# Performance work log

Measured on AMD Instinct MI355X. Metric: run time of the kernel, lower is better.

Reference implementation:

```python
import jax, jax.numpy as jnp
import numpy as np

N = 16384      # nodes per graph
E = 262144     # edges per graph
D_IN = 144     # number_of_labels(16) + 128
F1, F2, F3 = 128, 64, 32
K = 16         # tensor_neurons
BINS = 16
BOTTLE = 16


def gcn_conv(x, edge_index, W, b, n):
    """PyG-style GCNConv: D^-1/2 (A+I) D^-1/2 (x W) + b."""
    h = x @ W
    loops = jnp.arange(n)
    row = jnp.concatenate([edge_index[0], loops])
    col = jnp.concatenate([edge_index[1], loops])
    deg = jax.ops.segment_sum(jnp.ones_like(row, dtype=h.dtype), row, num_segments=n)
    dinv = jax.lax.rsqrt(jnp.maximum(deg, 1e-12))
    norm = dinv[row] * dinv[col]                 # [E+N]
    msg = h[col] * norm[:, None]                 # gather + scale
    out = jax.ops.segment_sum(msg, row, num_segments=n)  # scatter-add
    return out + b


def conv_pass(edge_index, x, W1, b1, W2, b2, W3, b3, n):
    x = jax.nn.relu(gcn_conv(x, edge_index, W1, b1, n))
    x = jax.nn.relu(gcn_conv(x, edge_index, W2, b2, n))
    return gcn_conv(x, edge_index, W3, b3, n)    # [N, F3]


def attention_pool(x, att_W):
    # global context -> tanh -> sigmoid node gates -> weighted sum
    tg = jnp.tanh(jnp.mean(x @ att_W, axis=0))   # [F3]
    gates = jax.nn.sigmoid(x @ tg)               # [N]
    return (x.T @ gates)[:, None]                # [F3, 1]


def tensor_network(e1, e2, tW, tWb, tb):
    # e1, e2: [F3, 1]
    s = (e1.T @ tW.reshape(F3, -1)).reshape(F3, K)
    s = s.T @ e2                                 # [K, 1]
    blk = tWb @ jnp.concatenate([e1, e2], axis=0)  # [K, 1]
    return jax.nn.relu(s + blk + tb)


def simgnn_forward(features_1, features_2, W1, b1, W2, b2, W3, b3,
                   att_W, tnet_W, tnet_Wb, tnet_bias, fc_W, fc_b, sc_W, sc_b,
                   edge_index_1, edge_index_2):
    af1 = conv_pass(edge_index_1, features_1, W1, b1, W2, b2, W3, b3, N)
    af2 = conv_pass(edge_index_2, features_2, W1, b1, W2, b2, W3, b3, N)

    # histogram of pairwise similarity scores (detached in original)
    sim = jax.lax.stop_gradient(af1 @ af2.T)     # [N, N] -- 1 GB fp32
    counts, _ = jnp.histogram(sim.reshape(-1), bins=BINS)
    hist = (counts.astype(features_1.dtype) / counts.sum()).reshape(1, BINS)

    p1 = attention_pool(af1, att_W)
    p2 = attention_pool(af2, att_W)
    scores = tensor_network(p1, p2, tnet_W, tnet_Wb, tnet_bias).T  # [1, K]
    scores = jnp.concatenate([scores, hist], axis=1).reshape(1, -1)  # [1, K+BINS]

    scores = jax.nn.relu(scores @ fc_W.T + fc_b)
    return jax.nn.sigmoid(scores @ sc_W.T + sc_b)  # [1, 1]


def setup_inputs() -> dict:
    key = jax.random.key(0)
    ks = jax.random.split(key, 20)
    g = lambda k, shp, s: (jax.random.normal(k, shp, dtype=jnp.float32) * s)
    return {
        "features_1": jax.random.normal(ks[0], (N, D_IN), dtype=jnp.float32),
        "features_2": jax.random.normal(ks[1], (N, D_IN), dtype=jnp.float32),
        "edge_index_1": jax.random.randint(ks[2], (2, E), 0, N, dtype=jnp.int32),
        "edge_index_2": jax.random.randint(ks[3], (2, E), 0, N, dtype=jnp.int32),
        "W1": g(ks[4], (D_IN, F1), 0.08), "b1": jnp.zeros((F1,), jnp.float32),
        "W2": g(ks[5], (F1, F2), 0.09), "b2": jnp.zeros((F2,), jnp.float32),
        "W3": g(ks[6], (F2, F3), 0.12), "b3": jnp.zeros((F3,), jnp.float32),
        "att_W": g(ks[7], (F3, F3), 0.17),
        "tnet_W": g(ks[8], (F3, F3, K), 0.05),
        "tnet_Wb": g(ks[9], (K, 2 * F3), 0.1),
        "tnet_bias": g(ks[10], (K, 1), 0.1),
        "fc_W": g(ks[11], (BOTTLE, K + BINS), 0.15),
        "fc_b": jnp.zeros((BOTTLE,), jnp.float32),
        "sc_W": g(ks[12], (1, BOTTLE), 0.2),
        "sc_b": jnp.zeros((1,), jnp.float32),
    }


def reference(features_1, features_2, edge_index_1, edge_index_2,
              W1, b1, W2, b2, W3, b3, att_W, tnet_W, tnet_Wb, tnet_bias,
              fc_W, fc_b, sc_W, sc_b):
    return simgnn_forward(features_1, features_2, W1, b1, W2, b2, W3, b3,
                          att_W, tnet_W, tnet_Wb, tnet_bias, fc_W, fc_b, sc_W, sc_b,
                          edge_index_1, edge_index_2)
```

## Files before the change

### kernel.cpp

```cpp
#include <hip/hip_runtime.h>
#include <hip/hip_bf16.h>
#include <math.h>

#define NN 16384
#define EE 262144
#define DIN 144
#define F1d 128
#define F2d 64
#define F3d 32

#define SIM_BLOCKS 1024

typedef __attribute__((ext_vector_type(8))) short bf16x8;
typedef __attribute__((ext_vector_type(4))) float f32x4;

__device__ __forceinline__ unsigned short f2bf(float f){
  unsigned u = __float_as_uint(f);
  unsigned r = (u + 0x7fffu + ((u >> 16) & 1u)) >> 16;
  return (unsigned short)r;
}

__global__ void prep_deg(const float* __restrict__ f0, const float* __restrict__ f1,
                         const float* __restrict__ W1, const float* __restrict__ W2,
                         const float* __restrict__ W3,
                         const int* __restrict__ ei0, const int* __restrict__ ei1,
                         unsigned short* __restrict__ Xb,
                         unsigned short* __restrict__ W1T,
                         unsigned short* __restrict__ W2T,
                         unsigned short* __restrict__ W3T,
                         int* __restrict__ deg){
  int b = blockIdx.x;
  int t = threadIdx.x;
  if (b < 5120){
    int g = (b >= 2560) ? 1 : 0;
    int bb = b - g * 2560;
    const float* F = g ? f1 : f0;
    int idx = bb * 256 + t;
    int i = idx / 40, q = idx % 40;
    ushort4 o;
    if (q < 36){
      float4 v = *(const float4*)(F + (size_t)i * DIN + q * 4);
      o.x = f2bf(v.x); o.y = f2bf(v.y); o.z = f2bf(v.z); o.w = f2bf(v.w);
    } else {
      o.x = 0; o.y = 0; o.z = 0; o.w = 0;
    }
    *(ushort4*)(Xb + ((size_t)g * NN + i) * 160 + q * 4) = o;
  } else if (b < 5240){
    int idx = (b - 5120) * 256 + t;
    if (idx < 20480){
      int f = idx / 160, k = idx % 160;
      W1T[idx] = (k < DIN) ? f2bf(W1[k * F1d + f]) : (unsigned short)0;
    } else if (idx < 28672){
      int r = idx - 20480; int f = r / 128, k = r % 128;
      W2T[r] = f2bf(W2[k * F2d + f]);
    } else if (idx < 30720){
      int r = idx - 28672; int f = r / 64, k = r % 64;
      W3T[r] = f2bf(W3[k * F3d + f]);
    }
  } else {
    int db = b - 5240;
    int g = db >> 10;
    const int* ei = g ? ei1 : ei0;
    int e = (db & 1023) * 256 + t;
    atomicAdd(&deg[g * NN + ei[e]], 1);
  }
}

__global__ void scan_kernel(const int* __restrict__ degb, int* __restrict__ rpb,
                            float* __restrict__ dinvb, int* __restrict__ curb){
  int g = blockIdx.x;
  const int* deg = degb + g * NN;
  int* rp = rpb + g * (NN + 1);
  float* dinv = dinvb + g * NN;
  int* cur = curb + g * NN;
  int t = threadIdx.x;
  int base = t * 16;
  int v[16]; int s = 0;
#pragma unroll
  for (int i = 0; i < 16; i++){ v[i] = deg[base + i]; s += v[i]; }
  int incl = s;
#pragma unroll
  for (int o = 1; o < 64; o <<= 1){
    int y = __shfl_up(incl, o, 64);
    if ((t & 63) >= o) incl += y;
  }
  __shared__ int wtot[16], woff[16];
  if ((t & 63) == 63) wtot[t >> 6] = incl;
  __syncthreads();
  if (t < 16){
    int x = wtot[t];
    int inc2 = x;
#pragma unroll
    for (int o = 1; o < 16; o <<= 1){
      int y = __shfl_up(inc2, o, 16);
      if (t >= o) inc2 += y;
    }
    woff[t] = inc2 - x;
  }
  __syncthreads();
  int excl = woff[t >> 6] + incl - s;
#pragma unroll
  for (int i = 0; i < 16; i++){
    rp[base + i] = excl;
    cur[base + i] = excl;
    dinv[base + i] = 1.0f / sqrtf((float)(v[i] + 1));
    excl += v[i];
  }
  if (t == 1023) rp[NN] = excl;
}

__global__ __attribute__((amdgpu_flat_work_group_size(256, 256), amdgpu_waves_per_eu(2, 2)))
void gemm1_fill(const unsigned short* __restrict__ A,
                const unsigned short* __restrict__ BT,
                const float* __restrict__ dinv,
                unsigned short* __restrict__ HS,
                const int* __restrict__ ei0, const int* __restrict__ ei1,
                int* __restrict__ cur, int* __restrict__ col){
  constexpr int KP = 160, FD = F1d, NT = FD / 32;
  int t = threadIdx.x;
  if (blockIdx.x < 256){
    int l = t & 63, w = t >> 6;
    int wr = w >> 1, wc = w & 1;
    int i0 = blockIdx.x * 128 + wr * 64;
    int j0 = wc * (FD / 2);
    int m = l & 15;
    int k0 = (l >> 4) * 8;
    int quad = l >> 4;

    f32x4 acc[4][NT];
#pragma unroll
    for (int u = 0; u < 4; u++)
#pragma unroll
      for (int v = 0; v < NT; v++)
        acc[u][v] = (f32x4){0.f, 0.f, 0.f, 0.f};

    for (int kk = 0; kk < KP; kk += 32){
      bf16x8 a[4], b[NT];
#pragma unroll
      for (int u = 0; u < 4; u++)
        a[u] = *(const bf16x8*)(A + (size_t)(i0 + u * 16 + m) * KP + kk + k0);
#pragma unroll
      for (int v = 0; v < NT; v++)
        b[v] = *(const bf16x8*)(BT + (size_t)(j0 + v * 16 + m) * KP + kk + k0);
#pragma unroll
      for (int u = 0; u < 4; u++)
#pragma unroll
        for (int v = 0; v < NT; v++)
          acc[u][v] = __builtin_amdgcn_mfma_f32_16x16x32_bf16(a[u], b[v], acc[u][v], 0, 0, 0);
    }

#pragma unroll
    for (int u = 0; u < 4; u++){
      float dv[4];
#pragma unroll
      for (int r = 0; r < 4; r++)
        dv[r] = dinv[i0 + u * 16 + quad * 4 + r];
#pragma unroll
      for (int v = 0; v < NT; v++){
#pragma unroll
        for (int r = 0; r < 4; r++){
          int row = i0 + u * 16 + quad * 4 + r;
          HS[(size_t)row * FD + j0 + v * 16 + m] = f2bf(acc[u][v][r] * dv[r]);
        }
      }
    }
  } else {
    int db = blockIdx.x - 256;
    int g = db >> 10;
    const int* ei = g ? ei1 : ei0;
    int e = (db & 1023) * 256 + t;
    int r = ei[e];
    int pos = atomicAdd(&cur[g * NN + r], 1);
    col[g * EE + pos] = ei[EE + e];
  }
}

__device__ __forceinline__ void acc8(float* acc, uint4 q){
  acc[0] += __uint_as_float(q.x << 16);
  acc[1] += __uint_as_float(q.x & 0xffff0000u);
  acc[2] += __uint_as_float(q.y << 16);
  acc[3] += __uint_as_float(q.y & 0xffff0000u);
  acc[4] += __uint_as_float(q.z << 16);
  acc[5] += __uint_as_float(q.z & 0xffff0000u);
  acc[6] += __uint_as_float(q.w << 16);
  acc[7] += __uint_as_float(q.w & 0xffff0000u);
}

template<int FD, int OUT>
__global__ __launch_bounds__(256)
void agg_gemm(const unsigned short* __restrict__ HS,
              const int* __restrict__ rp,
              const int* __restrict__ col,
              const float* __restrict__ dinv,
              const float* __restrict__ bias,
              const unsigned short* __restrict__ WT,
              unsigned short* __restrict__ HOUT){
  constexpr int TPN = FD / 8;
  constexpr int NPB = 256 / TPN;
  constexpr int NTt = OUT / 16;
  static_assert((NPB / 16) * NTt == 4, "wave tiling must cover 4 waves");
  __shared__ unsigned short Arow[NPB][FD + 8];

  int bid = blockIdx.x;
  int b8 = bid & 7;
  int g = b8 >> 2;
  int chunk = (bid >> 3) * 4 + (b8 & 3);
  int t = threadIdx.x;
  int f8 = t % TPN;
  int n = t / TPN;
  int i = chunk * NPB + n;
  const uint4* HS16 = (const uint4*)HS;
  size_t gb = (size_t)g * NN;
  float acc[8];
  {
    uint4 q = HS16[(gb + i) * TPN + f8];
    acc[0] = __uint_as_float(q.x << 16);
    acc[1] = __uint_as_float(q.x & 0xffff0000u);
    acc[2] = __uint_as_float(q.y << 16);
    acc[3] = __uint_as_float(q.y & 0xffff0000u);
    acc[4] = __uint_as_float(q.z << 16);
    acc[5] = __uint_as_float(q.z & 0xffff0000u);
    acc[6] = __uint_as_float(q.w << 16);
    acc[7] = __uint_as_float(q.w & 0xffff0000u);
  }
  int p0 = rp[g * (NN + 1) + i], p1 = rp[g * (NN + 1) + i + 1];
  const int* colg = col + (size_t)g * EE;
  int p = p0;
  for (; p + 8 <= p1; p += 8){
    int j0 = colg[p],     j1 = colg[p + 1], j2 = colg[p + 2], j3 = colg[p + 3];
    int j4 = colg[p + 4], j5 = colg[p + 5], j6 = colg[p + 6], j7 = colg[p + 7];
    uint4 q0 = HS16[(gb + j0) * TPN + f8];
    uint4 q1 = HS16[(gb + j1) * TPN + f8];
    uint4 q2 = HS16[(gb + j2) * TPN + f8];
    uint4 q3 = HS16[(gb + j3) * TPN + f8];
    uint4 q4 = HS16[(gb + j4) * TPN + f8];
    uint4 q5 = HS16[(gb + j5) * TPN + f8];
    uint4 q6 = HS16[(gb + j6) * TPN + f8];
    uint4 q7 = HS16[(gb + j7) * TPN + f8];
    acc8(acc, q0); acc8(acc, q1); acc8(acc, q2); acc8(acc, q3);
    acc8(acc, q4); acc8(acc, q5); acc8(acc, q6); acc8(acc, q7);
  }
  for (; p + 4 <= p1; p += 4){
    int j0 = colg[p], j1 = colg[p + 1], j2 = colg[p + 2], j3 = colg[p + 3];
    uint4 q0 = HS16[(gb + j0) * TPN + f8];
    uint4 q1 = HS16[(gb + j1) * TPN + f8];
    uint4 q2 = HS16[(gb + j2) * TPN + f8];
    uint4 q3 = HS16[(gb + j3) * TPN + f8];
    acc8(acc, q0); acc8(acc, q1); acc8(acc, q2); acc8(acc, q3);
  }
  for (; p + 2 <= p1; p += 2){
    int j0 = colg[p], j1 = colg[p + 1];
    uint4 q0 = HS16[(gb + j0) * TPN + f8];
    uint4 q1 = HS16[(gb + j1) * TPN + f8];
    acc8(acc, q0); acc8(acc, q1);
  }
  if (p < p1){
    uint4 q = HS16[(gb + colg[p]) * TPN + f8];
    acc8(acc, q);
  }
  float di = dinv[g * NN + i];
  float o[8];
#pragma unroll
  for (int k = 0; k < 8; k++)
    o[k] = fmaxf(di * acc[k] + bias[f8 * 8 + k], 0.f);
  uint4 qo;
  qo.x = (unsigned)f2bf(o[0]) | ((unsigned)f2bf(o[1]) << 16);
  qo.y = (unsigned)f2bf(o[2]) | ((unsigned)f2bf(o[3]) << 16);
  qo.z = (unsigned)f2bf(o[4]) | ((unsigned)f2bf(o[5]) << 16);
  qo.w = (unsigned)f2bf(o[6]) | ((unsigned)f2bf(o[7]) << 16);
  *(uint4*)&Arow[n][f8 * 8] = qo;
  __syncthreads();

  int l = t & 63, w = t >> 6;
  int m = l & 15, quad = l >> 4;
  int u = w / NTt, v = w % NTt;
  f32x4 facc = (f32x4){0.f, 0.f, 0.f, 0.f};
#pragma unroll
  for (int kk = 0; kk < FD; kk += 32){
    bf16x8 af = *(const bf16x8*)&Arow[u * 16 + m][kk + quad * 8];
    bf16x8 bf = *(const bf16x8*)(WT + (size_t)(v * 16 + m) * FD + kk + quad * 8);
    facc = __builtin_amdgcn_mfma_f32_16x16x32_bf16(af, bf, facc, 0, 0, 0);
  }
#pragma unroll
  for (int r = 0; r < 4; r++){
    int ig = chunk * NPB + u * 16 + quad * 4 + r;
    HOUT[((size_t)g * NN + ig) * OUT + v * 16 + m] = f2bf(dinv[g * NN + ig] * facc[r]);
  }
}

template<int FD, bool RELU, bool FINAL>
__global__ __launch_bounds__(256) void agg_kernel(const unsigned short* __restrict__ HS,
                                                  const int* __restrict__ rp,
                                                  const int* __restrict__ col,
                                                  const float* __restrict__ dinv,
                                                  const float* __restrict__ b,
                                                  unsigned short* __restrict__ OUTB,
                                                  float* __restrict__ cpart){
  constexpr int TPN = FD / 8;
  constexpr int NPB = 256 / TPN;
  int bid = blockIdx.x;
  int b8 = bid & 7;
  int g = b8 >> 2;
  int chunk = (bid >> 3) * 4 + (b8 & 3);
  int t = threadIdx.x;
  int f8 = t % TPN;
  int i = chunk * NPB + t / TPN;
  const uint4* HS16 = (const uint4*)HS;
  size_t gb = (size_t)g * NN;
  float acc[8];
  {
    uint4 q = HS16[(gb + i) * TPN + f8];
    acc[0] = __uint_as_float(q.x << 16);
    acc[1] = __uint_as_float(q.x & 0xffff0000u);
    acc[2] = __uint_as_float(q.y << 16);
    acc[3] = __uint_as_float(q.y & 0xffff0000u);
    acc[4] = __uint_as_float(q.z << 16);
    acc[5] = __uint_as_float(q.z & 0xffff0000u);
    acc[6] = __uint_as_float(q.w << 16);
    acc[7] = __uint_as_float(q.w & 0xffff0000u);
  }
  int p0 = rp[g * (NN + 1) + i], p1 = rp[g * (NN + 1) + i + 1];
  const int* colg = col + (size_t)g * EE;
  int p = p0;
  for (; p + 8 <= p1; p += 8){
    int j0 = colg[p],     j1 = colg[p + 1], j2 = colg[p + 2], j3 = colg[p + 3];
    int j4 = colg[p + 4], j5 = colg[p + 5], j6 = colg[p + 6], j7 = colg[p + 7];
    uint4 q0 = HS16[(gb + j0) * TPN + f8];
    uint4 q1 = HS16[(gb + j1) * TPN + f8];
    uint4 q2 = HS16[(gb + j2) * TPN + f8];
    uint4 q3 = HS16[(gb + j3) * TPN + f8];
    uint4 q4 = HS16[(gb + j4) * TPN + f8];
    uint4 q5 = HS16[(gb + j5) * TPN + f8];
    uint4 q6 = HS16[(gb + j6) * TPN + f8];
    uint4 q7 = HS16[(gb + j7) * TPN + f8];
    acc8(acc, q0); acc8(acc, q1); acc8(acc, q2); acc8(acc, q3);
    acc8(acc, q4); acc8(acc, q5); acc8(acc, q6); acc8(acc, q7);
  }
  for (; p + 4 <= p1; p += 4){
    int j0 = colg[p], j1 = colg[p + 1], j2 = colg[p + 2], j3 = colg[p + 3];
    uint4 q0 = HS16[(gb + j0) * TPN + f8];
    uint4 q1 = HS16[(gb + j1) * TPN + f8];
    uint4 q2 = HS16[(gb + j2) * TPN + f8];
    uint4 q3 = HS16[(gb + j3) * TPN + f8];
    acc8(acc, q0); acc8(acc, q1); acc8(acc, q2); acc8(acc, q3);
  }
  for (; p + 2 <= p1; p += 2){
    int j0 = colg[p], j1 = colg[p + 1];
    uint4 q0 = HS16[(gb + j0) * TPN + f8];
    uint4 q1 = HS16[(gb + j1) * TPN + f8];
    acc8(acc, q0);
    acc8(acc, q1);
  }
  if (p < p1){
    uint4 q = HS16[(gb + colg[p]) * TPN + f8];
    acc8(acc, q);
  }
  float di = dinv[g * NN + i];
  float o[8];
#pragma unroll
  for (int k = 0; k < 8; k++){
    o[k] = di * acc[k] + b[f8 * 8 + k];
    if (RELU) o[k] = fmaxf(o[k], 0.f);
  }
  uint4 qo;
  qo.x = (unsigned)f2bf(o[0]) | ((unsigned)f2bf(o[1]) << 16);
  qo.y = (unsigned)f2bf(o[2]) | ((unsigned)f2bf(o[3]) << 16);
  qo.z = (unsigned)f2bf(o[4]) | ((unsigned)f2bf(o[5]) << 16);
  qo.w = (unsigned)f2bf(o[6]) | ((unsigned)f2bf(o[7]) << 16);
  ((uint4*)OUTB)[(gb + i) * TPN + f8] = qo;
  if (FINAL){
    __shared__ float s[256][8];
#pragma unroll
    for (int k = 0; k < 8; k++) s[t][k] = o[k];
    __syncthreads();
    if (t < 32){
      float sum = 0.f;
#pragma unroll 8
      for (int n = 0; n < NPB; n++)
        sum += s[n * TPN + (t >> 3)][t & 7];
      cpart[((size_t)g * 256 + chunk) * 32 + t] = sum;
    }
  }
}

__global__ __attribute__((amdgpu_flat_work_group_size(256, 256), amdgpu_waves_per_eu(4, 4)))
void sim1_pool(const unsigned short* __restrict__ A,
               const unsigned short* __restrict__ B,
               float* __restrict__ pmm,
               const float* __restrict__ cpart,
               const float* __restrict__ attW,
               float* __restrict__ ppart){
  int t = threadIdx.x;
  if (blockIdx.x < SIM_BLOCKS){
    int l = t & 63, w = t >> 6;
    int wave_id = blockIdx.x * 4 + w;
    int istrip = wave_id >> 5;
    int jgrp = wave_id & 31;
    int i0 = istrip * 128;
    int m  = l & 15;
    int k0 = (l >> 4) * 8;

    bf16x8 a[8];
#pragma unroll
    for (int u = 0; u < 8; u++)
      a[u] = *(const bf16x8*)(A + (size_t)(i0 + u * 16 + m) * 32 + k0);

    float mn = 3.402823466e38f, mx = -3.402823466e38f;
    int j0 = jgrp * 512 + (istrip & 7) * 64;
    bf16x8 b[4];
#pragma unroll
    for (int v = 0; v < 4; v++)
      b[v] = *(const bf16x8*)(B + (size_t)(j0 + v * 16 + m) * 32 + k0);
#pragma unroll
    for (int u = 0; u < 8; u++)
#pragma unroll
      for (int v = 0; v < 4; v++){
        f32x4 z = {0.f, 0.f, 0.f, 0.f};
        f32x4 acc = __builtin_amdgcn_mfma_f32_16x16x32_bf16(a[u], b[v], z, 0, 0, 0);
        mn = fminf(fminf(acc[0], acc[1]), mn);
        mn = fminf(fminf(acc[2], acc[3]), mn);
        mx = fmaxf(fmaxf(acc[0], acc[1]), mx);
        mx = fmaxf(fmaxf(acc[2], acc[3]), mx);
      }
#pragma unroll
    for (int o = 32; o >= 1; o >>= 1){
      mn = fminf(mn, __shfl_xor(mn, o));
      mx = fmaxf(mx, __shfl_xor(mx, o));
    }
    __shared__ float wmn[4], wmx[4];
    if (l == 0){ wmn[w] = mn; wmx[w] = mx; }
    __syncthreads();
    if (t == 0){
      pmm[blockIdx.x * 2]     = fminf(fminf(wmn[0], wmn[1]), fminf(wmn[2], wmn[3]));
      pmm[blockIdx.x * 2 + 1] = fmaxf(fmaxf(wmx[0], wmx[1]), fmaxf(wmx[2], wmx[3]));
    }
  } else {
    __shared__ float red8[8][32];
    __shared__ float csl[32], tgl[32];
    __shared__ float s[16][32];
    int bid2 = blockIdx.x - SIM_BLOCKS;
    int g = bid2 >> 7;
    int xb = bid2 & 127;
    {
      int f = t & 31, part = t >> 5;
      float cs = 0.f;
      for (int b = part; b < 256; b += 8)
        cs += cpart[((size_t)g * 256 + b) * 32 + f];
      red8[part][f] = cs;
    }
    __syncthreads();
    if (t < 32){
      float cs = 0.f;
#pragma unroll
      for (int k = 0; k < 8; k++) cs += red8[k][t];
      csl[t] = cs * (1.f / (float)NN);
    }
    __syncthreads();
    if (t < 32){
      float acc = 0.f;
      for (int k = 0; k < 32; k++)
        acc += csl[k] * attW[k * 32 + t];
      tgl[t] = tanhf(acc);
    }
    __syncthreads();

    int f2 = t & 15, slot = t >> 4;
    float tg0 = tgl[f2 * 2], tg1 = tgl[f2 * 2 + 1];
    const unsigned* AFu = (const unsigned*)((const unsigned short*)A + (size_t)g * NN * 32);
    float a0 = 0.f, a1 = 0.f;
    for (int i = xb * 16 + slot; i < NN; i += 128 * 16){
      unsigned u = AFu[(size_t)i * 16 + f2];
      float lo = __uint_as_float(u << 16);
      float hi = __uint_as_float(u & 0xffff0000u);
      float d = lo * tg0 + hi * tg1;
#pragma unroll
      for (int o = 8; o >= 1; o >>= 1) d += __shfl_xor(d, o, 16);
      float gate = 1.f / (1.f + expf(-d));
      a0 += lo * gate;
      a1 += hi * gate;
    }
    s[slot][f2 * 2] = a0;
    s[slot][f2 * 2 + 1] = a1;
    __syncthreads();
    if (t < 32){
      float tot = 0.f;
#pragma unroll
      for (int k = 0; k < 16; k++) tot += s[k][t];
      ppart[((size_t)g * 128 + xb) * 32 + t] = tot;
    }
  }
}

__global__ __attribute__((amdgpu_flat_work_group_size(256, 256), amdgpu_waves_per_eu(4, 4)))
void sim_pass2(const unsigned short* __restrict__ A,
               const unsigned short* __restrict__ B,
               const float* __restrict__ pmm,
               unsigned* __restrict__ phist){
  __shared__ unsigned lh[4][16][64];
  __shared__ unsigned red[16][16];
  __shared__ float wmn[4], wmx[4], osc[2];
  int t = threadIdx.x;
  int l = t & 63, w = t >> 6;

  {
    float mn = 3.402823466e38f, mx = -3.402823466e38f;
#pragma unroll
    for (int k = 0; k < 4; k++){
      int b = t * 4 + k;
      mn = fminf(mn, pmm[b * 2]);
      mx = fmaxf(mx, pmm[b * 2 + 1]);
    }
#pragma unroll
    for (int o = 32; o >= 1; o >>= 1){
      mn = fminf(mn, __shfl_xor(mn, o));
      mx = fmaxf(mx, __shfl_xor(mx, o));
    }
    if (l == 0){ wmn[w] = mn; wmx[w] = mx; }
    __syncthreads();
    if (t == 0){
      float lo = fminf(fminf(wmn[0], wmn[1]), fminf(wmn[2], wmn[3]));
      float hi = fmaxf(fmaxf(wmx[0], wmx[1]), fmaxf(wmx[2], wmx[3]));
      float sc = (hi > lo) ? (16.f / (hi - lo)) : 0.f;
      osc[0] = -lo * sc;
      osc[1] = sc;
    }
    __syncthreads();
  }
  float off = osc[0], sc = osc[1];

  int wave_id = blockIdx.x * 4 + w;
  int istrip = wave_id >> 5;
  int jgrp = wave_id & 31;
  int i0 = istrip * 128;
  int m  = l & 15;
  int k0 = (l >> 4) * 8;

  unsigned* myslot = &lh[w][0][l];
#pragma unroll
  for (int q = 0; q < 16; q++) myslot[q * 64] = 0u;

  bf16x8 a[8];
#pragma unroll
  for (int u = 0; u < 8; u++)
    a[u] = *(const bf16x8*)(A + (size_t)(i0 + u * 16 + m) * 32 + k0);

  int j0 = jgrp * 512 + (istrip & 7) * 64;
  bf16x8 b[4];
#pragma unroll
  for (int v = 0; v < 4; v++)
    b[v] = *(const bf16x8*)(B + (size_t)(j0 + v * 16 + m) * 32 + k0);
#pragma unroll
  for (int u = 0; u < 8; u++)
#pragma unroll
    for (int v = 0; v < 4; v++){
      f32x4 z = {0.f, 0.f, 0.f, 0.f};
      f32x4 acc = __builtin_amdgcn_mfma_f32_16x16x32_bf16(a[u], b[v], z, 0, 0, 0);
#pragma unroll
      for (int r = 0; r < 4; r++){
        int idx = (int)__builtin_amdgcn_fmed3f(fmaf(acc[r], sc, off), 0.f, 15.f);
        atomicAdd(&myslot[idx * 64], 1u);
      }
    }

  __syncthreads();
  int bin = t & 15, part = t >> 4;
  unsigned s = 0;
#pragma unroll
  for (int ww = 0; ww < 4; ww++)
#pragma unroll
    for (int lc = 0; lc < 4; lc++)
      s += lh[ww][bin][part * 4 + lc];
  red[part][bin] = s;
  __syncthreads();
  if (t < 16){
    unsigned tot = 0;
#pragma unroll
    for (int p = 0; p < 16; p++) tot += red[p][t];
    phist[blockIdx.x * 16 + t] = tot;
  }
}

__global__ void final_kernel(const float* __restrict__ ppart, const unsigned* __restrict__ phist,
                             const float* __restrict__ tW, const float* __restrict__ tWb,
                             const float* __restrict__ tb,
                             const float* __restrict__ fcW, const float* __restrict__ fcb,
                             const float* __restrict__ scW, const float* __restrict__ scb,
                             float* __restrict__ out){
  __shared__ float e[2][32], v32[32], uu[16], hn[16];
  __shared__ unsigned htmp[256];
  __shared__ float4 accL[256];
  int t = threadIdx.x;

  if (t < 64){
    int g = t >> 5, f = t & 31;
    float s = 0.f;
    for (int b = 0; b < 128; b++)
      s += ppart[((size_t)g * 128 + b) * 32 + f];
    e[g][f] = s;
  }
  {
    int bin = t & 15;
    unsigned hs = 0;
    for (int b = t >> 4; b < SIM_BLOCKS; b += 16)
      hs += phist[b * 16 + bin];
    htmp[t] = hs;
  }
  __syncthreads();

  if (t < 16){
    unsigned c = 0;
#pragma unroll
    for (int p = 0; p < 16; p++) c += htmp[p * 16 + t];
    hn[t] = (float)c;
  }

  const float4* tw4 = (const float4*)tW;
  float4 acc = {0.f, 0.f, 0.f, 0.f};
#pragma unroll
  for (int i = 0; i < 16; i++){
    int idx = t + 256 * i;
    int pair = idx >> 2;
    float coef = e[0][pair >> 5] * e[1][pair & 31];
    float4 w4 = tw4[idx];
    acc.x += coef * w4.x; acc.y += coef * w4.y;
    acc.z += coef * w4.z; acc.w += coef * w4.w;
  }
  accL[t] = acc;
  __syncthreads();

  if (t < 16){
    int q = t >> 2, r = t & 3;
    float s = 0.f;
    for (int j = 0; j < 64; j++){
      float4 a4 = accL[q + 4 * j];
      s += (r == 0) ? a4.x : (r == 1) ? a4.y : (r == 2) ? a4.z : a4.w;
    }
    float blk = 0.f;
    for (int a = 0; a < 32; a++) blk += tWb[t * 64 + a] * e[0][a];
    for (int b = 0; b < 32; b++) blk += tWb[t * 64 + 32 + b] * e[1][b];
    float rr = s + blk + tb[t];
    v32[t] = rr > 0.f ? rr : 0.f;
  }
  __syncthreads();

  if (t < 16){
    float tot = 0.f;
#pragma unroll
    for (int i = 0; i < 16; i++) tot += hn[i];
    float inv = 1.f / tot;
    float s = fcb[t];
    for (int i = 0; i < 16; i++) s += fcW[t * 32 + i] * v32[i];
    for (int i = 0; i < 16; i++) s += fcW[t * 32 + 16 + i] * (hn[i] * inv);
    uu[t] = s > 0.f ? s : 0.f;
  }
  __syncthreads();
  if (t == 0){
    float s = scb[0];
    for (int i = 0; i < 16; i++) s += scW[i] * uu[i];
    out[0] = 1.f / (1.f + expf(-s));
  }
}

extern "C" void kernel_launch(void* const* d_in, const int* in_sizes, int n_in,
                              void* d_out, int out_size, void* d_ws, size_t ws_size,
                              hipStream_t stream){
  const float* feat0 = (const float*)d_in[0];
  const float* feat1 = (const float*)d_in[1];
  const int*   ei0   = (const int*)d_in[2];
  const int*   ei1   = (const int*)d_in[3];
  const float* W1  = (const float*)d_in[4];
  const float* b1  = (const float*)d_in[5];
  const float* W2  = (const float*)d_in[6];
  const float* b2  = (const float*)d_in[7];
  const float* W3  = (const float*)d_in[8];
  const float* b3  = (const float*)d_in[9];
  const float* attW = (const float*)d_in[10];
  const float* tW  = (const float*)d_in[11];
  const float* tWb = (const float*)d_in[12];
  const float* tb  = (const float*)d_in[13];
  const float* fcW = (const float*)d_in[14];
  const float* fcb = (const float*)d_in[15];
  const float* scW = (const float*)d_in[16];
  const float* scb = (const float*)d_in[17];

  char* w = (char*)d_ws;
  size_t o = 0;
  auto alloc = [&](size_t bytes)->char*{
    char* p = w + o; o += (bytes + 255) & ~(size_t)255; return p;
  };
  int* deg   = (int*)alloc((size_t)2 * NN * 4);
  int* rp    = (int*)alloc((size_t)2 * (NN + 1) * 4);
  int* cur   = (int*)alloc((size_t)2 * NN * 4);
  int* col   = (int*)alloc((size_t)2 * EE * 4);
  float* dinv = (float*)alloc((size_t)2 * NN * 4);
  unsigned short* Xb  = (unsigned short*)alloc((size_t)2 * NN * 160 * 2);
  unsigned short* W1T = (unsigned short*)alloc((size_t)128 * 160 * 2);
  unsigned short* W2T = (unsigned short*)alloc((size_t)64 * 128 * 2);
  unsigned short* W3T = (unsigned short*)alloc((size_t)32 * 64 * 2);
  unsigned short* hs  = (unsigned short*)alloc((size_t)2 * NN * F1d * 2);
  unsigned short* ab1 = (unsigned short*)alloc((size_t)2 * NN * F1d * 2);
  unsigned short* ab2 = (unsigned short*)alloc((size_t)2 * NN * F2d * 2);
  unsigned short* afb = (unsigned short*)alloc((size_t)2 * NN * F3d * 2);
  float* cpart = (float*)alloc((size_t)2 * 256 * 32 * 4);
  float* ppart = (float*)alloc((size_t)2 * 128 * 32 * 4);
  float* pmm   = (float*)alloc((size_t)SIM_BLOCKS * 2 * 4);
  unsigned* phist = (unsigned*)alloc((size_t)SIM_BLOCKS * 16 * 4);

  hipMemsetAsync(deg, 0, (size_t)2 * NN * 4, stream);
  prep_deg<<<7288, 256, 0, stream>>>(feat0, feat1, W1, W2, W3, ei0, ei1,
                                     Xb, W1T, W2T, W3T, deg);
  scan_kernel<<<2, 1024, 0, stream>>>(deg, rp, dinv, cur);

  gemm1_fill<<<2304, 256, 0, stream>>>(Xb, W1T, dinv, hs, ei0, ei1, cur, col);
  agg_gemm<F1d, F2d><<<2 * NN / 16, 256, 0, stream>>>(hs, rp, col, dinv, b1, W2T, ab1);
  agg_gemm<F2d, F3d><<<2 * NN / 32, 256, 0, stream>>>(ab1, rp, col, dinv, b2, W3T, ab2);
  agg_kernel<F3d, false, true><<<2 * NN / 64, 256, 0, stream>>>(ab2, rp, col, dinv, b3, afb, cpart);

  const unsigned short* afb0 = afb;
  const unsigned short* afb1 = afb + (size_t)NN * F3d;
  sim1_pool<<<SIM_BLOCKS + 256, 256, 0, stream>>>(afb0, afb1, pmm, cpart, attW, ppart);
  sim_pass2<<<SIM_BLOCKS, 256, 0, stream>>>(afb0, afb1, pmm, phist);

  final_kernel<<<1, 256, 0, stream>>>(ppart, phist, tW, tWb, tb,
                                      fcW, fcb, scW, scb, (float*)d_out);
}
```

Baseline: 245.6 us.

## Merge pre-processing and similarity stages into persistent kernels with grid barriers

Replaces the separate prep, scan, gemm1/fill kernels with one persistent 1024-block kernel, and the final aggregation, similarity min/max, pooling, histogram and final kernels with a second persistent kernel. Stages are separated by software grid barriers built on atomic counters in workspace, which removes several kernel launches and their gaps. The scan now runs with 256 threads over four passes instead of 1024 threads. It depends on all 1024 blocks being co-resident, since it is launched normally rather than cooperatively; if they are not, the barriers deadlock. Idle blocks also spin during the serial scan and final stages.

```diff
diff --git a/kernel.cpp b/kernel.cpp
--- a/kernel.cpp
+++ b/kernel.cpp
@@ -10,6 +10,7 @@
 #define F3d 32
 
 #define SIM_BLOCKS 1024
+#define COOP_GRID 1024
 
 typedef __attribute__((ext_vector_type(8))) short bf16x8;
 typedef __attribute__((ext_vector_type(4))) float f32x4;
@@ -20,7 +21,20 @@
   return (unsigned short)r;
 }
 
-__global__ void prep_deg(const float* __restrict__ f0, const float* __restrict__ f1,
+__device__ __forceinline__ void gbar(int* c, int target){
+  __syncthreads();
+  if (threadIdx.x == 0){
+    __builtin_amdgcn_fence(__ATOMIC_RELEASE, "agent");
+    __hip_atomic_fetch_add(c, 1, __ATOMIC_RELAXED, __HIP_MEMORY_SCOPE_AGENT);
+    while (__hip_atomic_load(c, __ATOMIC_RELAXED, __HIP_MEMORY_SCOPE_AGENT) < target)
+      __builtin_amdgcn_s_sleep(2);
+    __builtin_amdgcn_fence(__ATOMIC_ACQUIRE, "agent");
+  }
+  __syncthreads();
+}
+
+__device__ __forceinline__ void prep_unit(int b,
+                         const float* __restrict__ f0, const float* __restrict__ f1,
                          const float* __restrict__ W1, const float* __restrict__ W2,
                          const float* __restrict__ W3,
                          const int* __restrict__ ei0, const int* __restrict__ ei1,
@@ -29,7 +43,6 @@
                          unsigned short* __restrict__ W2T,
                          unsigned short* __restrict__ W3T,
                          int* __restrict__ deg){
-  int b = blockIdx.x;
   int t = threadIdx.x;
   if (b < 5120){
     int g = (b >= 2560) ? 1 : 0;
@@ -66,112 +79,142 @@
   }
 }
 
-__global__ void scan_kernel(const int* __restrict__ degb, int* __restrict__ rpb,
-                            float* __restrict__ dinvb, int* __restrict__ curb){
-  int g = blockIdx.x;
+__device__ __forceinline__ void scan_unit(int g, const int* __restrict__ degb,
+                                          int* __restrict__ rpb,
+                                          float* __restrict__ dinvb,
+                                          int* __restrict__ curb){
   const int* deg = degb + g * NN;
   int* rp = rpb + g * (NN + 1);
   float* dinv = dinvb + g * NN;
   int* cur = curb + g * NN;
-  int t = threadIdx.x;
-  int base = t * 16;
-  int v[16]; int s = 0;
-#pragma unroll
-  for (int i = 0; i < 16; i++){ v[i] = deg[base + i]; s += v[i]; }
-  int incl = s;
-#pragma unroll
-  for (int o = 1; o < 64; o <<= 1){
-    int y = __shfl_up(incl, o, 64);
-    if ((t & 63) >= o) incl += y;
-  }
-  __shared__ int wtot[16], woff[16];
-  if ((t & 63) == 63) wtot[t >> 6] = incl;
-  __syncthreads();
-  if (t < 16){
-    int x = wtot[t];
-    int inc2 = x;
-#pragma unroll
-    for (int o = 1; o < 16; o <<= 1){
-      int y = __shfl_up(inc2, o, 16);
-      if (t >= o) inc2 += y;
-    }
-    woff[t] = inc2 - x;
-  }
-  __syncthreads();
-  int excl = woff[t >> 6] + incl - s;
-#pragma unroll
-  for (int i = 0; i < 16; i++){
-    rp[base + i] = excl;
-    cur[base + i] = excl;
-    dinv[base + i] = 1.0f / sqrtf((float)(v[i] + 1));
-    excl += v[i];
-  }
-  if (t == 1023) rp[NN] = excl;
-}
-
-__global__ __attribute__((amdgpu_flat_work_group_size(256, 256), amdgpu_waves_per_eu(2, 2)))
-void gemm1_fill(const unsigned short* __restrict__ A,
+  __shared__ int wtot[4];
+  int t = threadIdx.x;
+  int carry = 0;
+  for (int pass = 0; pass < 4; pass++){
+    int base = pass * 4096 + t * 16;
+    int v[16]; int s = 0;
+#pragma unroll
+    for (int i = 0; i < 16; i++){ v[i] = deg[base + i]; s += v[i]; }
+    int incl = s;
+#pragma unroll
+    for (int o = 1; o < 64; o <<= 1){
+      int y = __shfl_up(incl, o, 64);
+      if ((t & 63) >= o) incl += y;
+    }
+    if ((t & 63) == 63) wtot[t >> 6] = incl;
+    __syncthreads();
+    int w4 = t >> 6;
+    int woff = 0;
+    if (w4 > 0) woff += wtot[0];
+    if (w4 > 1) woff += wtot[1];
+    if (w4 > 2) woff += wtot[2];
+    int btot = wtot[0] + wtot[1] + wtot[2] + wtot[3];
+    int excl = carry + woff + incl - s;
+#pragma unroll
+    for (int i = 0; i < 16; i++){
+      rp[base + i] = excl;
+      cur[base + i] = excl;
+      dinv[base + i] = 1.0f / sqrtf((float)(v[i] + 1));
+      excl += v[i];
+    }
+    carry += btot;
+    __syncthreads();
+  }
+  if (t == 0) rp[NN] = carry;
+}
+
+__device__ __forceinline__ void gemm1_unit(int u,
+                const unsigned short* __restrict__ A,
                 const unsigned short* __restrict__ BT,
                 const float* __restrict__ dinv,
-                unsigned short* __restrict__ HS,
+                unsigned short* __restrict__ HS){
+  constexpr int KP = 160, FD = F1d, NT = FD / 32;
+  int t = threadIdx.x;
+  int l = t & 63, w = t >> 6;
+  int wr = w >> 1, wc = w & 1;
+  int i0 = u * 128 + wr * 64;
+  int j0 = wc * (FD / 2);
+  int m = l & 15;
+  int k0 = (l >> 4) * 8;
+  int quad = l >> 4;
+
+  f32x4 acc[4][NT];
+#pragma unroll
+  for (int uu = 0; uu < 4; uu++)
+#pragma unroll
+    for (int v = 0; v < NT; v++)
+      acc[uu][v] = (f32x4){0.f, 0.f, 0.f, 0.f};
+
+  for (int kk = 0; kk < KP; kk += 32){
+    bf16x8 a[4], b[NT];
+#pragma unroll
+    for (int uu = 0; uu < 4; uu++)
+      a[uu] = *(const bf16x8*)(A + (size_t)(i0 + uu * 16 + m) * KP + kk + k0);
+#pragma unroll
+    for (int v = 0; v < NT; v++)
+      b[v] = *(const bf16x8*)(BT + (size_t)(j0 + v * 16 + m) * KP + kk + k0);
+#pragma unroll
+    for (int uu = 0; uu < 4; uu++)
+#pragma unroll
+      for (int v = 0; v < NT; v++)
+        acc[uu][v] = __builtin_amdgcn_mfma_f32_16x16x32_bf16(a[uu], b[v], acc[uu][v], 0, 0, 0);
+  }
+
+#pragma unroll
+  for (int uu = 0; uu < 4; uu++){
+    float dv[4];
+#pragma unroll
+    for (int r = 0; r < 4; r++)
+      dv[r] = dinv[i0 + uu * 16 + quad * 4 + r];
+#pragma unroll
+    for (int v = 0; v < NT; v++){
+#pragma unroll
+      for (int r = 0; r < 4; r++){
+        int row = i0 + uu * 16 + quad * 4 + r;
+        HS[(size_t)row * FD + j0 + v * 16 + m] = f2bf(acc[uu][v][r] * dv[r]);
+      }
+    }
+  }
+}
+
+__device__ __forceinline__ void fill_unit(int db,
                 const int* __restrict__ ei0, const int* __restrict__ ei1,
                 int* __restrict__ cur, int* __restrict__ col){
-  constexpr int KP = 160, FD = F1d, NT = FD / 32;
-  int t = threadIdx.x;
-  if (blockIdx.x < 256){
-    int l = t & 63, w = t >> 6;
-    int wr = w >> 1, wc = w & 1;
-    int i0 = blockIdx.x * 128 + wr * 64;
-    int j0 = wc * (FD / 2);
-    int m = l & 15;
-    int k0 = (l >> 4) * 8;
-    int quad = l >> 4;
-
-    f32x4 acc[4][NT];
-#pragma unroll
-    for (int u = 0; u < 4; u++)
-#pragma unroll
-      for (int v = 0; v < NT; v++)
-        acc[u][v] = (f32x4){0.f, 0.f, 0.f, 0.f};
-
-    for (int kk = 0; kk < KP; kk += 32){
-      bf16x8 a[4], b[NT];
-#pragma unroll
-      for (int u = 0; u < 4; u++)
-        a[u] = *(const bf16x8*)(A + (size_t)(i0 + u * 16 + m) * KP + kk + k0);
-#pragma unroll
-      for (int v = 0; v < NT; v++)
-        b[v] = *(const bf16x8*)(BT + (size_t)(j0 + v * 16 + m) * KP + kk + k0);
-#pragma unroll
-      for (int u = 0; u < 4; u++)
-#pragma unroll
-        for (int v = 0; v < NT; v++)
-          acc[u][v] = __builtin_amdgcn_mfma_f32_16x16x32_bf16(a[u], b[v], acc[u][v], 0, 0, 0);
-    }
-
-#pragma unroll
-    for (int u = 0; u < 4; u++){
-      float dv[4];
-#pragma unroll
-      for (int r = 0; r < 4; r++)
-        dv[r] = dinv[i0 + u * 16 + quad * 4 + r];
-#pragma unroll
-      for (int v = 0; v < NT; v++){
-#pragma unroll
-        for (int r = 0; r < 4; r++){
-          int row = i0 + u * 16 + quad * 4 + r;
-          HS[(size_t)row * FD + j0 + v * 16 + m] = f2bf(acc[u][v][r] * dv[r]);
-        }
-      }
-    }
-  } else {
-    int db = blockIdx.x - 256;
-    int g = db >> 10;
-    const int* ei = g ? ei1 : ei0;
-    int e = (db & 1023) * 256 + t;
-    int r = ei[e];
-    int pos = atomicAdd(&cur[g * NN + r], 1);
-    col[g * EE + pos] = ei[EE + e];
+  int t = threadIdx.x;
+  int g = db >> 10;
+  const int* ei = g ? ei1 : ei0;
+  int e = (db & 1023) * 256 + t;
+  int r = ei[e];
+  int pos = atomicAdd(&cur[g * NN + r], 1);
+  col[g * EE + pos] = ei[EE + e];
+}
+
+__global__ __launch_bounds__(256, 4)
+void pre_coop(const float* __restrict__ f0, const float* __restrict__ f1,
+              const float* __restrict__ W1, const float* __restrict__ W2,
+              const float* __restrict__ W3,
+              const int* __restrict__ ei0, const int* __restrict__ ei1,
+              unsigned short* __restrict__ Xb,
+              unsigned short* __restrict__ W1T,
+              unsigned short* __restrict__ W2T,
+              unsigned short* __restrict__ W3T,
+              int* __restrict__ deg, int* __restrict__ rp,
+              float* __restrict__ dinv, int* __restrict__ cur,
+              int* __restrict__ col, unsigned short* __restrict__ hs,
+              int* __restrict__ bar){
+  for (int u = blockIdx.x; u < 7288; u += COOP_GRID)
+    prep_unit(u, f0, f1, W1, W2, W3, ei0, ei1, Xb, W1T, W2T, W3T, deg);
+  gbar(&bar[0], COOP_GRID);
+  if (blockIdx.x < 2)
+    scan_unit(blockIdx.x, deg, rp, dinv, cur);
+  gbar(&bar[1], COOP_GRID);
+  {
+    int b = blockIdx.x;
+    if (b < 256) gemm1_unit(b, Xb, W1T, dinv, hs);
+    else         fill_unit(b - 256, ei0, ei1, cur, col);
+    int u2 = b + 1024;
+    fill_unit(u2 - 256, ei0, ei1, cur, col);
+    if (b < 256) fill_unit(b + 2048 - 256, ei0, ei1, cur, col);
   }
 }
 
@@ -288,17 +331,18 @@
   }
 }
 
-template<int FD, bool RELU, bool FINAL>
-__global__ __launch_bounds__(256) void agg_kernel(const unsigned short* __restrict__ HS,
-                                                  const int* __restrict__ rp,
-                                                  const int* __restrict__ col,
-                                                  const float* __restrict__ dinv,
-                                                  const float* __restrict__ b,
-                                                  unsigned short* __restrict__ OUTB,
-                                                  float* __restrict__ cpart){
+__device__ __forceinline__ void agg3_unit(int bid,
+                const unsigned short* __restrict__ HS,
+                const int* __restrict__ rp,
+                const int* __restrict__ col,
+                const float* __restrict__ dinv,
+                const float* __restrict__ b,
+                unsigned short* __restrict__ OUTB,
+                float* __restrict__ cpart){
+  constexpr int FD = F3d;
   constexpr int TPN = FD / 8;
   constexpr int NPB = 256 / TPN;
-  int bid = blockIdx.x;
+  __shared__ float s3[256][8];
   int b8 = bid & 7;
   int g = b8 >> 2;
   int chunk = (bid >> 3) * 4 + (b8 & 3);
@@ -348,8 +392,7 @@
     int j0 = colg[p], j1 = colg[p + 1];
     uint4 q0 = HS16[(gb + j0) * TPN + f8];
     uint4 q1 = HS16[(gb + j1) * TPN + f8];
-    acc8(acc, q0);
-    acc8(acc, q1);
+    acc8(acc, q0); acc8(acc, q1);
   }
   if (p < p1){
     uint4 q = HS16[(gb + colg[p]) * TPN + f8];
@@ -358,141 +401,138 @@
   float di = dinv[g * NN + i];
   float o[8];
 #pragma unroll
-  for (int k = 0; k < 8; k++){
+  for (int k = 0; k < 8; k++)
     o[k] = di * acc[k] + b[f8 * 8 + k];
-    if (RELU) o[k] = fmaxf(o[k], 0.f);
-  }
   uint4 qo;
   qo.x = (unsigned)f2bf(o[0]) | ((unsigned)f2bf(o[1]) << 16);
   qo.y = (unsigned)f2bf(o[2]) | ((unsigned)f2bf(o[3]) << 16);
   qo.z = (unsigned)f2bf(o[4]) | ((unsigned)f2bf(o[5]) << 16);
   qo.w = (unsigned)f2bf(o[6]) | ((unsigned)f2bf(o[7]) << 16);
   ((uint4*)OUTB)[(gb + i) * TPN + f8] = qo;
-  if (FINAL){
-    __shared__ float s[256][8];
-#pragma unroll
-    for (int k = 0; k < 8; k++) s[t][k] = o[k];
-    __syncthreads();
-    if (t < 32){
-      float sum = 0.f;
+#pragma unroll
+  for (int k = 0; k < 8; k++) s3[t][k] = o[k];
+  __syncthreads();
+  if (t < 32){
+    float sum = 0.f;
 #pragma unroll 8
-      for (int n = 0; n < NPB; n++)
-        sum += s[n * TPN + (t >> 3)][t & 7];
-      cpart[((size_t)g * 256 + chunk) * 32 + t] = sum;
-    }
-  }
-}
-
-__global__ __attribute__((amdgpu_flat_work_group_size(256, 256), amdgpu_waves_per_eu(4, 4)))
-void sim1_pool(const unsigned short* __restrict__ A,
+    for (int n = 0; n < NPB; n++)
+      sum += s3[n * TPN + (t >> 3)][t & 7];
+    cpart[((size_t)g * 256 + chunk) * 32 + t] = sum;
+  }
+}
+
+__device__ __forceinline__ void sim_mm_unit(int u,
+               const unsigned short* __restrict__ A,
                const unsigned short* __restrict__ B,
-               float* __restrict__ pmm,
+               float* __restrict__ pmm){
+  __shared__ float wmn[4], wmx[4];
+  int t = threadIdx.x;
+  int l = t & 63, w = t >> 6;
+  int wave_id = u * 4 + w;
+  int istrip = wave_id >> 5;
+  int jgrp = wave_id & 31;
+  int i0 = istrip * 128;
+  int m  = l & 15;
+  int k0 = (l >> 4) * 8;
+
+  bf16x8 a[8];
+#pragma unroll
+  for (int uu = 0; uu < 8; uu++)
+    a[uu] = *(const bf16x8*)(A + (size_t)(i0 + uu * 16 + m) * 32 + k0);
+
+  float mn = 3.402823466e38f, mx = -3.402823466e38f;
+  int j0 = jgrp * 512 + (istrip & 7) * 64;
+  bf16x8 b[4];
+#pragma unroll
+  for (int v = 0; v < 4; v++)
+    b[v] = *(const bf16x8*)(B + (size_t)(j0 + v * 16 + m) * 32 + k0);
+#pragma unroll
+  for (int uu = 0; uu < 8; uu++)
+#pragma unroll
+    for (int v = 0; v < 4; v++){
+      f32x4 z = {0.f, 0.f, 0.f, 0.f};
+      f32x4 acc = __builtin_amdgcn_mfma_f32_16x16x32_bf16(a[uu], b[v], z, 0, 0, 0);
+      mn = fminf(fminf(acc[0], acc[1]), mn);
+      mn = fminf(fminf(acc[2], acc[3]), mn);
+      mx = fmaxf(fmaxf(acc[0], acc[1]), mx);
+      mx = fmaxf(fmaxf(acc[2], acc[3]), mx);
+    }
+#pragma unroll
+  for (int o = 32; o >= 1; o >>= 1){
+    mn = fminf(mn, __shfl_xor(mn, o));
+    mx = fmaxf(mx, __shfl_xor(mx, o));
+  }
+  if (l == 0){ wmn[w] = mn; wmx[w] = mx; }
+  __syncthreads();
+  if (t == 0){
+    pmm[u * 2]     = fminf(fminf(wmn[0], wmn[1]), fminf(wmn[2], wmn[3]));
+    pmm[u * 2 + 1] = fmaxf(fmaxf(wmx[0], wmx[1]), fmaxf(wmx[2], wmx[3]));
+  }
+  __syncthreads();
+}
+
+__device__ __forceinline__ void pool_unit(int bid2,
+               const unsigned short* __restrict__ A,
                const float* __restrict__ cpart,
                const float* __restrict__ attW,
                float* __restrict__ ppart){
-  int t = threadIdx.x;
-  if (blockIdx.x < SIM_BLOCKS){
-    int l = t & 63, w = t >> 6;
-    int wave_id = blockIdx.x * 4 + w;
-    int istrip = wave_id >> 5;
-    int jgrp = wave_id & 31;
-    int i0 = istrip * 128;
-    int m  = l & 15;
-    int k0 = (l >> 4) * 8;
-
-    bf16x8 a[8];
-#pragma unroll
-    for (int u = 0; u < 8; u++)
-      a[u] = *(const bf16x8*)(A + (size_t)(i0 + u * 16 + m) * 32 + k0);
-
-    float mn = 3.402823466e38f, mx = -3.402823466e38f;
-    int j0 = jgrp * 512 + (istrip & 7) * 64;
-    bf16x8 b[4];
-#pragma unroll
-    for (int v = 0; v < 4; v++)
-      b[v] = *(const bf16x8*)(B + (size_t)(j0 + v * 16 + m) * 32 + k0);
-#pragma unroll
-    for (int u = 0; u < 8; u++)
-#pragma unroll
-      for (int v = 0; v < 4; v++){
-        f32x4 z = {0.f, 0.f, 0.f, 0.f};
-        f32x4 acc = __builtin_amdgcn_mfma_f32_16x16x32_bf16(a[u], b[v], z, 0, 0, 0);
-        mn = fminf(fminf(acc[0], acc[1]), mn);
-        mn = fminf(fminf(acc[2], acc[3]), mn);
-        mx = fmaxf(fmaxf(acc[0], acc[1]), mx);
-        mx = fmaxf(fmaxf(acc[2], acc[3]), mx);
-      }
-#pragma unroll
-    for (int o = 32; o >= 1; o >>= 1){
-      mn = fminf(mn, __shfl_xor(mn, o));
-      mx = fmaxf(mx, __shfl_xor(mx, o));
-    }
-    __shared__ float wmn[4], wmx[4];
-    if (l == 0){ wmn[w] = mn; wmx[w] = mx; }
-    __syncthreads();
-    if (t == 0){
-      pmm[blockIdx.x * 2]     = fminf(fminf(wmn[0], wmn[1]), fminf(wmn[2], wmn[3]));
-      pmm[blockIdx.x * 2 + 1] = fmaxf(fmaxf(wmx[0], wmx[1]), fmaxf(wmx[2], wmx[3]));
-    }
-  } else {
-    __shared__ float red8[8][32];
-    __shared__ float csl[32], tgl[32];
-    __shared__ float s[16][32];
-    int bid2 = blockIdx.x - SIM_BLOCKS;
-    int g = bid2 >> 7;
-    int xb = bid2 & 127;
-    {
-      int f = t & 31, part = t >> 5;
-      float cs = 0.f;
-      for (int b = part; b < 256; b += 8)
-        cs += cpart[((size_t)g * 256 + b) * 32 + f];
-      red8[part][f] = cs;
-    }
-    __syncthreads();
-    if (t < 32){
-      float cs = 0.f;
-#pragma unroll
-      for (int k = 0; k < 8; k++) cs += red8[k][t];
-      csl[t] = cs * (1.f / (float)NN);
-    }
-    __syncthreads();
-    if (t < 32){
-      float acc = 0.f;
-      for (int k = 0; k < 32; k++)
-        acc += csl[k] * attW[k * 32 + t];
-      tgl[t] = tanhf(acc);
-    }
-    __syncthreads();
-
-    int f2 = t & 15, slot = t >> 4;
-    float tg0 = tgl[f2 * 2], tg1 = tgl[f2 * 2 + 1];
-    const unsigned* AFu = (const unsigned*)((const unsigned short*)A + (size_t)g * NN * 32);
-    float a0 = 0.f, a1 = 0.f;
-    for (int i = xb * 16 + slot; i < NN; i += 128 * 16){
-      unsigned u = AFu[(size_t)i * 16 + f2];
-      float lo = __uint_as_float(u << 16);
-      float hi = __uint_as_float(u & 0xffff0000u);
-      float d = lo * tg0 + hi * tg1;
-#pragma unroll
-      for (int o = 8; o >= 1; o >>= 1) d += __shfl_xor(d, o, 16);
-      float gate = 1.f / (1.f + expf(-d));
-      a0 += lo * gate;
-      a1 += hi * gate;
-    }
-    s[slot][f2 * 2] = a0;
-    s[slot][f2 * 2 + 1] = a1;
-    __syncthreads();
-    if (t < 32){
-      float tot = 0.f;
-#pragma unroll
-      for (int k = 0; k < 16; k++) tot += s[k][t];
-      ppart[((size_t)g * 128 + xb) * 32 + t] = tot;
-    }
-  }
-}
-
-__global__ __attribute__((amdgpu_flat_work_group_size(256, 256), amdgpu_waves_per_eu(4, 4)))
-void sim_pass2(const unsigned short* __restrict__ A,
+  __shared__ float red8[8][32];
+  __shared__ float csl[32], tgl[32];
+  __shared__ float sp[16][32];
+  int t = threadIdx.x;
+  int g = bid2 >> 7;
+  int xb = bid2 & 127;
+  {
+    int f = t & 31, part = t >> 5;
+    float cs = 0.f;
+    for (int b = part; b < 256; b += 8)
+      cs += cpart[((size_t)g * 256 + b) * 32 + f];
+    red8[part][f] = cs;
+  }
+  __syncthreads();
+  if (t < 32){
+    float cs = 0.f;
+#pragma unroll
+    for (int k = 0; k < 8; k++) cs += red8[k][t];
+    csl[t] = cs * (1.f / (float)NN);
+  }
+  __syncthreads();
+  if (t < 32){
+    float acc = 0.f;
+    for (int k = 0; k < 32; k++)
+      acc += csl[k] * attW[k * 32 + t];
+    tgl[t] = tanhf(acc);
+  }
+  __syncthreads();
+
+  int f2 = t & 15, slot = t >> 4;
+  float tg0 = tgl[f2 * 2], tg1 = tgl[f2 * 2 + 1];
+  const unsigned* AFu = (const unsigned*)(A + (size_t)g * NN * 32);
+  float a0 = 0.f, a1 = 0.f;
+  for (int i = xb * 16 + slot; i < NN; i += 128 * 16){
+    unsigned uu = AFu[(size_t)i * 16 + f2];
+    float lo = __uint_as_float(uu << 16);
+    float hi = __uint_as_float(uu & 0xffff0000u);
+    float d = lo * tg0 + hi * tg1;
+#pragma unroll
+    for (int o = 8; o >= 1; o >>= 1) d += __shfl_xor(d, o, 16);
+    float gate = 1.f / (1.f + expf(-d));
+    a0 += lo * gate;
+    a1 += hi * gate;
+  }
+  sp[slot][f2 * 2] = a0;
+  sp[slot][f2 * 2 + 1] = a1;
+  __syncthreads();
+  if (t < 32){
+    float tot = 0.f;
+#pragma unroll
+    for (int k = 0; k < 16; k++) tot += sp[k][t];
+    ppart[((size_t)g * 128 + xb) * 32 + t] = tot;
+  }
+}
+
+__device__ __forceinline__ void bin_unit(int u,
+               const unsigned short* __restrict__ A,
                const unsigned short* __restrict__ B,
                const float* __restrict__ pmm,
                unsigned* __restrict__ phist){
@@ -528,7 +568,7 @@
   }
   float off = osc[0], sc = osc[1];
 
-  int wave_id = blockIdx.x * 4 + w;
+  int wave_id = u * 4 + w;
   int istrip = wave_id >> 5;
   int jgrp = wave_id & 31;
   int i0 = istrip * 128;
@@ -541,8 +581,8 @@
 
   bf16x8 a[8];
 #pragma unroll
-  for (int u = 0; u < 8; u++)
-    a[u] = *(const bf16x8*)(A + (size_t)(i0 + u * 16 + m) * 32 + k0);
+  for (int uu = 0; uu < 8; uu++)
+    a[uu] = *(const bf16x8*)(A + (size_t)(i0 + uu * 16 + m) * 32 + k0);
 
   int j0 = jgrp * 512 + (istrip & 7) * 64;
   bf16x8 b[4];
@@ -550,11 +590,11 @@
   for (int v = 0; v < 4; v++)
     b[v] = *(const bf16x8*)(B + (size_t)(j0 + v * 16 + m) * 32 + k0);
 #pragma unroll
-  for (int u = 0; u < 8; u++)
+  for (int uu = 0; uu < 8; uu++)
 #pragma unroll
     for (int v = 0; v < 4; v++){
       f32x4 z = {0.f, 0.f, 0.f, 0.f};
-      f32x4 acc = __builtin_amdgcn_mfma_f32_16x16x32_bf16(a[u], b[v], z, 0, 0, 0);
+      f32x4 acc = __builtin_amdgcn_mfma_f32_16x16x32_bf16(a[uu], b[v], z, 0, 0, 0);
 #pragma unroll
       for (int r = 0; r < 4; r++){
         int idx = (int)__builtin_amdgcn_fmed3f(fmaf(acc[r], sc, off), 0.f, 15.f);
@@ -576,17 +616,19 @@
     unsigned tot = 0;
 #pragma unroll
     for (int p = 0; p < 16; p++) tot += red[p][t];
-    phist[blockIdx.x * 16 + t] = tot;
-  }
-}
-
-__global__ void final_kernel(const float* __restrict__ ppart, const unsigned* __restrict__ phist,
+    phist[u * 16 + t] = tot;
+  }
+  __syncthreads();
+}
+
+__device__ __forceinline__ void final_unit(const float* __restrict__ ppart,
+                             const unsigned* __restrict__ phist,
                              const float* __restrict__ tW, const float* __restrict__ tWb,
                              const float* __restrict__ tb,
                              const float* __restrict__ fcW, const float* __restrict__ fcb,
                              const float* __restrict__ scW, const float* __restrict__ scb,
                              float* __restrict__ out){
-  __shared__ float e[2][32], v32[32], uu[16], hn[16];
+  __shared__ float e[2][32], v32[32], uu16[16], hn[16];
   __shared__ unsigned htmp[256];
   __shared__ float4 accL[256];
   int t = threadIdx.x;
@@ -651,14 +693,41 @@
     float s = fcb[t];
     for (int i = 0; i < 16; i++) s += fcW[t * 32 + i] * v32[i];
     for (int i = 0; i < 16; i++) s += fcW[t * 32 + 16 + i] * (hn[i] * inv);
-    uu[t] = s > 0.f ? s : 0.f;
+    uu16[t] = s > 0.f ? s : 0.f;
   }
   __syncthreads();
   if (t == 0){
     float s = scb[0];
-    for (int i = 0; i < 16; i++) s += scW[i] * uu[i];
+    for (int i = 0; i < 16; i++) s += scW[i] * uu16[i];
     out[0] = 1.f / (1.f + expf(-s));
   }
+}
+
+__global__ __launch_bounds__(256, 4)
+void sim_coop(const unsigned short* __restrict__ hs3,
+              const int* __restrict__ rp, const int* __restrict__ col,
+              const float* __restrict__ dinv, const float* __restrict__ b3,
+              unsigned short* __restrict__ afb, float* __restrict__ cpart,
+              const float* __restrict__ attW, float* __restrict__ ppart,
+              float* __restrict__ pmm, unsigned* __restrict__ phist,
+              const float* __restrict__ tW, const float* __restrict__ tWb,
+              const float* __restrict__ tb,
+              const float* __restrict__ fcW, const float* __restrict__ fcb,
+              const float* __restrict__ scW, const float* __restrict__ scb,
+              float* __restrict__ out, int* __restrict__ bar){
+  const unsigned short* afb0 = afb;
+  const unsigned short* afb1 = afb + (size_t)NN * F3d;
+  if (blockIdx.x < 512)
+    agg3_unit(blockIdx.x, hs3, rp, col, dinv, b3, afb, cpart);
+  gbar(&bar[2], COOP_GRID);
+  sim_mm_unit(blockIdx.x, afb0, afb1, pmm);
+  if (blockIdx.x < 256)
+    pool_unit(blockIdx.x, afb, cpart, attW, ppart);
+  gbar(&bar[3], COOP_GRID);
+  bin_unit(blockIdx.x, afb0, afb1, pmm, phist);
+  gbar(&bar[4], COOP_GRID);
+  if (blockIdx.x == 0)
+    final_unit(ppart, phist, tW, tWb, tb, fcW, fcb, scW, scb, out);
 }
 
 extern "C" void kernel_launch(void* const* d_in, const int* in_sizes, int n_in,
@@ -689,6 +758,7 @@
     char* p = w + o; o += (bytes + 255) & ~(size_t)255; return p;
   };
   int* deg   = (int*)alloc((size_t)2 * NN * 4);
+  int* bar   = (int*)alloc(256);
   int* rp    = (int*)alloc((size_t)2 * (NN + 1) * 4);
   int* cur   = (int*)alloc((size_t)2 * NN * 4);
   int* col   = (int*)alloc((size_t)2 * EE * 4);
@@ -706,21 +776,17 @@
   float* pmm   = (float*)alloc((size_t)SIM_BLOCKS * 2 * 4);
   unsigned* phist = (unsigned*)alloc((size_t)SIM_BLOCKS * 16 * 4);
 
-  hipMemsetAsync(deg, 0, (size_t)2 * NN * 4, stream);
-  prep_deg<<<7288, 256, 0, stream>>>(feat0, feat1, W1, W2, W3, ei0, ei1,
-                                     Xb, W1T, W2T, W3T, deg);
-  scan_kernel<<<2, 1024, 0, stream>>>(deg, rp, dinv, cur);
-
-  gemm1_fill<<<2304, 256, 0, stream>>>(Xb, W1T, dinv, hs, ei0, ei1, cur, col);
+  hipMemsetAsync(deg, 0, (size_t)2 * NN * 4 + 256, stream);
+
+  pre_coop<<<COOP_GRID, 256, 0, stream>>>(feat0, feat1, W1, W2, W3, ei0, ei1,
+                                          Xb, W1T, W2T, W3T,
+                                          deg, rp, dinv, cur, col, hs, bar);
+
   agg_gemm<F1d, F2d><<<2 * NN / 16, 256, 0, stream>>>(hs, rp, col, dinv, b1, W2T, ab1);
   agg_gemm<F2d, F3d><<<2 * NN / 32, 256, 0, stream>>>(ab1, rp, col, dinv, b2, W3T, ab2);
-  agg_kernel<F3d, false, true><<<2 * NN / 64, 256, 0, stream>>>(ab2, rp, col, dinv, b3, afb, cpart);
-
-  const unsigned short* afb0 = afb;
-  const unsigned short* afb1 = afb + (size_t)NN * F3d;
-  sim1_pool<<<SIM_BLOCKS + 256, 256, 0, stream>>>(afb0, afb1, pmm, cpart, attW, ppart);
-  sim_pass2<<<SIM_BLOCKS, 256, 0, stream>>>(afb0, afb1, pmm, phist);
-
-  final_kernel<<<1, 256, 0, stream>>>(ppart, phist, tW, tWb, tb,
-                                      fcW, fcb, scW, scb, (float*)d_out);
-}
+
+  sim_coop<<<COOP_GRID, 256, 0, stream>>>(ab2, rp, col, dinv, b3, afb, cpart,
+                                          attW, ppart, pmm, phist,
+                                          tW, tWb, tb, fcW, fcb, scW, scb,
+                                          (float*)d_out, bar);
+}
```

Result: slower. 566.3 us (+130.6%).
